# Optimization experiments

Measured on AMD Instinct MI355X. Metric: run time of the kernel, lower is better.

Reference implementation:

```python
import jax, jax.numpy as jnp
import numpy as np

HEAD_NUM = 16
SCALE = 1.0 / np.sqrt(HEAD_NUM)  # source divides by sqrt(head_num), not head_dim
MASK_VAL = -10000000.0


def setup_inputs() -> dict:
    key = jax.random.key(0)
    kq, kk, kv = jax.random.split(key, 3)
    shape = (2, 16, 2048, 64)  # [B, H, L, D]
    Q = jax.random.normal(kq, shape, dtype=jnp.float32)
    K = jax.random.normal(kk, shape, dtype=jnp.float32)
    V = jax.random.normal(kv, shape, dtype=jnp.float32)
    return {"Q": Q, "K": K, "V": V}


def reference(Q, K, V):
    L = Q.shape[-2]
    # [B, H, L, M] attention logits, scaled by 1/sqrt(head_num)
    logits = jnp.einsum('bhld,bhmd->bhlm', Q, K) * SCALE
    # causal mask: strictly-upper triangle gets -1e7 (additive, as in source)
    mask = jnp.triu(jnp.ones((L, L), dtype=logits.dtype), 1) * MASK_VAL
    logits = logits + mask[None, None, :, :]
    weights = jax.nn.softmax(logits, axis=-1)
    return jnp.einsum('bhlm,bhmd->bhld', weights, V)
```

## Files before the change

### kernel.cpp

```cpp
#include <hip/hip_runtime.h>
#include <hip/hip_bf16.h>

#define BM 128
#define BN 64
#define HD 64
#define LQ 2048
#define SD 72

typedef __attribute__((ext_vector_type(8))) short short8;
typedef __attribute__((ext_vector_type(4))) float f32x4;

#define QSCALE 0.360673760222241f

static __device__ __forceinline__ unsigned pk2(float a, float b) {
    union { __hip_bfloat162 h2; unsigned u; } c;
    c.h2 = __float22bfloat162_rn(make_float2(a, b));
    return c.u;
}

__global__ __launch_bounds__(512, 4)
void fa_fwd(const float* __restrict__ Qg,
            const float* __restrict__ Kg,
            const float* __restrict__ Vg,
            float* __restrict__ Og) {
    __shared__ unsigned short sQ[BM][SD];
    __shared__ unsigned short sK[2][BN][SD];
    __shared__ unsigned short sVt[2][HD][SD];
    __shared__ unsigned short sP[8][16][SD];

    const int t    = threadIdx.x;
    const int w    = t >> 6;
    const int lane = t & 63;
    const int qd   = lane >> 4;
    const int l    = lane & 15;

    const int bx  = blockIdx.x;
    const int idx = (bx >> 5) & 7;
    const int qt  = (bx & 256) ? idx : (15 - idx);
    const int bh  = bx & 31;
    const int q0  = qt * BM;

    const size_t base = (size_t)bh * (LQ * HD);
    const float* Qp = Qg + base + (size_t)q0 * HD;
    const float* Kp = Kg + base;
    const float* Vp = Vg + base;

    const int r0 = t >> 4;
    const int c4 = (t & 15) * 4;
    const int RA = w * 4;

#pragma unroll
    for (int p = 0; p < 4; ++p) {
        const int r = p * 32 + r0;
        const float4 v = *(const float4*)(Qp + (size_t)r * HD + c4);
        uint2 u;
        u.x = pk2(v.x * QSCALE, v.y * QSCALE);
        u.y = pk2(v.z * QSCALE, v.w * QSCALE);
        *(uint2*)&sQ[r][c4] = u;
    }

    float4 kA, kB, vA, vB;

    auto issue = [&](int kv0) {
        kA = *(const float4*)(Kp + (size_t)(kv0 + r0) * HD + c4);
        kB = *(const float4*)(Kp + (size_t)(kv0 + 32 + r0) * HD + c4);
        vA = *(const float4*)(Vp + (size_t)(kv0 + RA + qd) * HD + c4);
        vB = *(const float4*)(Vp + (size_t)(kv0 + 32 + RA + qd) * HD + c4);
    };

    auto vstore = [&](float4 vf, int R, int buf) {
        float e0 = vf.x, e1 = vf.y, e2 = vf.z, e3 = vf.w;
        float s0 = (qd & 2) ? e0 : e2;
        float s1 = (qd & 2) ? e1 : e3;
        s0 = __shfl_xor(s0, 32); s1 = __shfl_xor(s1, 32);
        if (qd & 2) { e0 = s0; e1 = s1; } else { e2 = s0; e3 = s1; }
        s0 = (qd & 1) ? e0 : e1;
        s1 = (qd & 1) ? e2 : e3;
        s0 = __shfl_xor(s0, 16); s1 = __shfl_xor(s1, 16);
        if (qd & 1) { e0 = s0; e2 = s1; } else { e1 = s0; e3 = s1; }
        const int d   = c4 + qd;
        const int col = ((((R >> 3) ^ (d >> 3)) & 7) << 3) | (R & 7);
        uint2 u; u.x = pk2(e0, e1); u.y = pk2(e2, e3);
        *(uint2*)&sVt[buf][d][col] = u;
    };

    auto commit = [&](int buf) {
        { uint2 u; u.x = pk2(kA.x, kA.y); u.y = pk2(kA.z, kA.w);
          *(uint2*)&sK[buf][r0][c4] = u; }
        { uint2 u; u.x = pk2(kB.x, kB.y); u.y = pk2(kB.z, kB.w);
          *(uint2*)&sK[buf][32 + r0][c4] = u; }
        vstore(vA, RA, buf);
        vstore(vB, 32 + RA, buf);
    };

    f32x4 accO[4];
#pragma unroll
    for (int mt = 0; mt < 4; ++mt) accO[mt] = (f32x4){0.f, 0.f, 0.f, 0.f};
    float lsum = 0.f;

    const int qrow  = q0 + w * 16 + l;
    const int qminw = q0 + w * 16;
    const int qmaxw = qminw + 15;
    const int n_it  = (q0 + BM) / BN;

    issue(0);
    commit(0);

    for (int it = 0; it < n_it; ++it) {
        const int kv0 = it * BN;
        const int buf = it & 1;
        __syncthreads();
        const bool more = (it + 1 < n_it);
        if (more) issue(kv0 + BN);

        if (kv0 <= qmaxw) {
            f32x4 accS[4];
#pragma unroll
            for (int mt = 0; mt < 4; ++mt) accS[mt] = (f32x4){0.f, 0.f, 0.f, 0.f};
#pragma unroll
            for (int ks = 0; ks < 2; ++ks) {
                const int ko = ks * 32 + qd * 8;
                const short8 bq = *(const short8*)&sQ[w * 16 + l][ko];
#pragma unroll
                for (int mt = 0; mt < 4; ++mt) {
                    const short8 ak = *(const short8*)&sK[buf][mt * 16 + l][ko];
                    accS[mt] = __builtin_amdgcn_mfma_f32_16x16x32_bf16(ak, bq, accS[mt], 0, 0, 0);
                }
            }

            if (kv0 + BN - 1 > qminw) {
#pragma unroll
                for (int mt = 0; mt < 4; ++mt) {
                    const int kvr = kv0 + mt * 16 + qd * 4;
#pragma unroll
                    for (int r = 0; r < 4; ++r)
                        if (kvr + r > qrow) accS[mt][r] = -1e30f;
                }
            }

#pragma unroll
            for (int mt = 0; mt < 4; ++mt) {
#pragma unroll
                for (int r = 0; r < 4; ++r) {
                    const float p = __builtin_amdgcn_exp2f(accS[mt][r]);
                    accS[mt][r] = p;
                    lsum += p;
                }
                uint2 u;
                u.x = pk2(accS[mt][0], accS[mt][1]);
                u.y = pk2(accS[mt][2], accS[mt][3]);
                *(uint2*)&sP[w][l][mt * 16 + qd * 4] = u;
            }
            asm volatile("s_waitcnt lgkmcnt(0)" ::: "memory");

            const int h = l >> 3;
#pragma unroll
            for (int ks = 0; ks < 2; ++ks) {
                const int ko = ks * 32 + qd * 8;
                const short8 bp = *(const short8*)&sP[w][l][ko];
#pragma unroll
                for (int mt = 0; mt < 4; ++mt) {
                    const int row = mt * 16 + l;
                    const int col = (((ks * 4 + qd) ^ (2 * mt + h)) & 7) << 3;
                    const short8 av = *(const short8*)&sVt[buf][row][col];
                    accO[mt] = __builtin_amdgcn_mfma_f32_16x16x32_bf16(av, bp, accO[mt], 0, 0, 0);
                }
            }
        }

        if (more) commit(buf ^ 1);
    }

    lsum += __shfl_xor(lsum, 16);
    lsum += __shfl_xor(lsum, 32);
    const float inv = 1.0f / lsum;
    float* Op = Og + base + (size_t)qrow * HD;
#pragma unroll
    for (int mt = 0; mt < 4; ++mt) {
        float4 o;
        o.x = accO[mt][0] * inv; o.y = accO[mt][1] * inv;
        o.z = accO[mt][2] * inv; o.w = accO[mt][3] * inv;
        *(float4*)(Op + mt * 16 + qd * 4) = o;
    }
}

extern "C" void kernel_launch(void* const* d_in, const int* in_sizes, int n_in,
                              void* d_out, int out_size, void* d_ws, size_t ws_size,
                              hipStream_t stream) {
    const float* Q = (const float*)d_in[0];
    const float* K = (const float*)d_in[1];
    const float* V = (const float*)d_in[2];
    float* O = (float*)d_out;
    fa_fwd<<<dim3(512), dim3(512), 0, stream>>>(Q, K, V, O);
}
```

Before: 124.2 us.

## Switch to 32x32x16 MFMA with 4 waves and Q in registers

```diff
diff --git a/kernel.cpp b/kernel.cpp
--- a/kernel.cpp
+++ b/kernel.cpp
@@ -5,12 +5,10 @@
 #define BN 64
 #define HD 64
 #define LQ 2048
-#define SD 72
+#define QSCALE 0.360673760222241f
 
 typedef __attribute__((ext_vector_type(8))) short short8;
-typedef __attribute__((ext_vector_type(4))) float f32x4;
-
-#define QSCALE 0.360673760222241f
+typedef __attribute__((ext_vector_type(16))) float f32x16;
 
 static __device__ __forceinline__ unsigned pk2(float a, float b) {
     union { __hip_bfloat162 h2; unsigned u; } c;
@@ -18,21 +16,24 @@
     return c.u;
 }
 
-__global__ __launch_bounds__(512, 4)
+static __device__ __forceinline__ int swz(int row, int oct) {
+    return (((row >> 3) ^ row) & 7) ^ oct;
+}
+
+__global__ __launch_bounds__(256, 3)
 void fa_fwd(const float* __restrict__ Qg,
             const float* __restrict__ Kg,
             const float* __restrict__ Vg,
             float* __restrict__ Og) {
-    __shared__ unsigned short sQ[BM][SD];
-    __shared__ unsigned short sK[2][BN][SD];
-    __shared__ unsigned short sVt[2][HD][SD];
-    __shared__ unsigned short sP[8][16][SD];
+    __shared__ unsigned short sK[2][BN][HD];
+    __shared__ unsigned short sVt[2][HD][BN];
+    __shared__ unsigned short sP[4][32][BN];
 
     const int t    = threadIdx.x;
     const int w    = t >> 6;
     const int lane = t & 63;
-    const int qd   = lane >> 4;
-    const int l    = lane & 15;
+    const int h    = lane >> 5;
+    const int l    = lane & 31;
 
     const int bx  = blockIdx.x;
     const int idx = (bx >> 5) & 7;
@@ -41,67 +42,80 @@
     const int q0  = qt * BM;
 
     const size_t base = (size_t)bh * (LQ * HD);
-    const float* Qp = Qg + base + (size_t)q0 * HD;
     const float* Kp = Kg + base;
     const float* Vp = Vg + base;
 
-    const int r0 = t >> 4;
-    const int c4 = (t & 15) * 4;
-    const int RA = w * 4;
-
-#pragma unroll
-    for (int p = 0; p < 4; ++p) {
-        const int r = p * 32 + r0;
-        const float4 v = *(const float4*)(Qp + (size_t)r * HD + c4);
-        uint2 u;
-        u.x = pk2(v.x * QSCALE, v.y * QSCALE);
-        u.y = pk2(v.z * QSCALE, v.w * QSCALE);
-        *(uint2*)&sQ[r][c4] = u;
+    const int qrow = q0 + w * 32 + l;
+
+    short8 bq[4];
+    {
+        const float* qp = Qg + base + (size_t)qrow * HD;
+#pragma unroll
+        for (int ks = 0; ks < 4; ++ks) {
+            const float4 a = *(const float4*)(qp + ks * 16 + h * 8);
+            const float4 b = *(const float4*)(qp + ks * 16 + h * 8 + 4);
+            union { short8 s; uint4 u; } cv;
+            cv.u.x = pk2(a.x * QSCALE, a.y * QSCALE);
+            cv.u.y = pk2(a.z * QSCALE, a.w * QSCALE);
+            cv.u.z = pk2(b.x * QSCALE, b.y * QSCALE);
+            cv.u.w = pk2(b.z * QSCALE, b.w * QSCALE);
+            bq[ks] = cv.s;
+        }
     }
 
-    float4 kA, kB, vA, vB;
-
+    const int kr   = t >> 4;
+    const int kc   = (t & 15) * 4;
+    const int ko   = (t & 15) >> 1;
+    const int koff = kc & 7;
+    const int vl   = lane & 15;
+    const int vqd  = lane >> 4;
+
+    float4 kf[4], vf[4];
     auto issue = [&](int kv0) {
-        kA = *(const float4*)(Kp + (size_t)(kv0 + r0) * HD + c4);
-        kB = *(const float4*)(Kp + (size_t)(kv0 + 32 + r0) * HD + c4);
-        vA = *(const float4*)(Vp + (size_t)(kv0 + RA + qd) * HD + c4);
-        vB = *(const float4*)(Vp + (size_t)(kv0 + 32 + RA + qd) * HD + c4);
+#pragma unroll
+        for (int p = 0; p < 4; ++p)
+            kf[p] = *(const float4*)(Kp + (size_t)(kv0 + p * 16 + kr) * HD + kc);
+#pragma unroll
+        for (int p = 0; p < 4; ++p)
+            vf[p] = *(const float4*)(Vp + (size_t)(kv0 + p * 16 + w * 4 + vqd) * HD + vl * 4);
     };
 
-    auto vstore = [&](float4 vf, int R, int buf) {
-        float e0 = vf.x, e1 = vf.y, e2 = vf.z, e3 = vf.w;
-        float s0 = (qd & 2) ? e0 : e2;
-        float s1 = (qd & 2) ? e1 : e3;
-        s0 = __shfl_xor(s0, 32); s1 = __shfl_xor(s1, 32);
-        if (qd & 2) { e0 = s0; e1 = s1; } else { e2 = s0; e3 = s1; }
-        s0 = (qd & 1) ? e0 : e1;
-        s1 = (qd & 1) ? e2 : e3;
-        s0 = __shfl_xor(s0, 16); s1 = __shfl_xor(s1, 16);
-        if (qd & 1) { e0 = s0; e2 = s1; } else { e1 = s0; e3 = s1; }
-        const int d   = c4 + qd;
-        const int col = ((((R >> 3) ^ (d >> 3)) & 7) << 3) | (R & 7);
-        uint2 u; u.x = pk2(e0, e1); u.y = pk2(e2, e3);
-        *(uint2*)&sVt[buf][d][col] = u;
+    auto commit = [&](int buf) {
+#pragma unroll
+        for (int p = 0; p < 4; ++p) {
+            const int r = p * 16 + kr;
+            uint2 u; u.x = pk2(kf[p].x, kf[p].y); u.y = pk2(kf[p].z, kf[p].w);
+            *(uint2*)&sK[buf][r][swz(r, ko) * 8 + koff] = u;
+        }
+#pragma unroll
+        for (int p = 0; p < 4; ++p) {
+            float e0 = vf[p].x, e1 = vf[p].y, e2 = vf[p].z, e3 = vf[p].w;
+            float s0 = (vqd & 2) ? e0 : e2;
+            float s1 = (vqd & 2) ? e1 : e3;
+            s0 = __shfl_xor(s0, 32); s1 = __shfl_xor(s1, 32);
+            if (vqd & 2) { e0 = s0; e1 = s1; } else { e2 = s0; e3 = s1; }
+            s0 = (vqd & 1) ? e0 : e1;
+            s1 = (vqd & 1) ? e2 : e3;
+            s0 = __shfl_xor(s0, 16); s1 = __shfl_xor(s1, 16);
+            if (vqd & 1) { e0 = s0; e2 = s1; } else { e1 = s0; e3 = s1; }
+            const int d = vl * 4 + vqd;
+            const int R = p * 16 + w * 4;
+            uint2 u; u.x = pk2(e0, e1); u.y = pk2(e2, e3);
+            *(uint2*)&sVt[buf][d][swz(d, R >> 3) * 8 + (R & 4)] = u;
+        }
     };
 
-    auto commit = [&](int buf) {
-        { uint2 u; u.x = pk2(kA.x, kA.y); u.y = pk2(kA.z, kA.w);
-          *(uint2*)&sK[buf][r0][c4] = u; }
-        { uint2 u; u.x = pk2(kB.x, kB.y); u.y = pk2(kB.z, kB.w);
-          *(uint2*)&sK[buf][32 + r0][c4] = u; }
-        vstore(vA, RA, buf);
-        vstore(vB, 32 + RA, buf);
-    };
-
-    f32x4 accO[4];
-#pragma unroll
-    for (int mt = 0; mt < 4; ++mt) accO[mt] = (f32x4){0.f, 0.f, 0.f, 0.f};
+    f32x16 accO[2];
+#pragma unroll
+    for (int mt = 0; mt < 2; ++mt)
+#pragma unroll
+        for (int i = 0; i < 16; ++i) accO[mt][i] = 0.f;
     float lsum = 0.f;
 
-    const int qrow  = q0 + w * 16 + l;
-    const int qminw = q0 + w * 16;
-    const int qmaxw = qminw + 15;
+    const int qminw = q0 + w * 32;
+    const int qmaxw = qminw + 31;
     const int n_it  = (q0 + BM) / BN;
+    const int swq   = ((l >> 3) ^ l) & 7;
 
     issue(0);
     commit(0);
@@ -114,74 +128,75 @@
         if (more) issue(kv0 + BN);
 
         if (kv0 <= qmaxw) {
-            f32x4 accS[4];
-#pragma unroll
-            for (int mt = 0; mt < 4; ++mt) accS[mt] = (f32x4){0.f, 0.f, 0.f, 0.f};
-#pragma unroll
-            for (int ks = 0; ks < 2; ++ks) {
-                const int ko = ks * 32 + qd * 8;
-                const short8 bq = *(const short8*)&sQ[w * 16 + l][ko];
-#pragma unroll
-                for (int mt = 0; mt < 4; ++mt) {
-                    const short8 ak = *(const short8*)&sK[buf][mt * 16 + l][ko];
-                    accS[mt] = __builtin_amdgcn_mfma_f32_16x16x32_bf16(ak, bq, accS[mt], 0, 0, 0);
+            f32x16 accS[2];
+#pragma unroll
+            for (int mt = 0; mt < 2; ++mt)
+#pragma unroll
+                for (int i = 0; i < 16; ++i) accS[mt][i] = 0.f;
+#pragma unroll
+            for (int ks = 0; ks < 4; ++ks) {
+#pragma unroll
+                for (int mt = 0; mt < 2; ++mt) {
+                    const int row = mt * 32 + l;
+                    const short8 ak = *(const short8*)&sK[buf][row][swz(row, 2 * ks + h) * 8];
+                    accS[mt] = __builtin_amdgcn_mfma_f32_32x32x16_bf16(ak, bq[ks], accS[mt], 0, 0, 0);
                 }
             }
 
             if (kv0 + BN - 1 > qminw) {
 #pragma unroll
-                for (int mt = 0; mt < 4; ++mt) {
-                    const int kvr = kv0 + mt * 16 + qd * 4;
-#pragma unroll
-                    for (int r = 0; r < 4; ++r)
-                        if (kvr + r > qrow) accS[mt][r] = -1e30f;
+                for (int mt = 0; mt < 2; ++mt)
+#pragma unroll
+                    for (int g = 0; g < 4; ++g)
+#pragma unroll
+                        for (int r = 0; r < 4; ++r)
+                            if (kv0 + mt * 32 + g * 8 + h * 4 + r > qrow)
+                                accS[mt][g * 4 + r] = -1e30f;
+            }
+
+#pragma unroll
+            for (int mt = 0; mt < 2; ++mt)
+#pragma unroll
+                for (int g = 0; g < 4; ++g) {
+                    const float p0 = __builtin_amdgcn_exp2f(accS[mt][g * 4 + 0]);
+                    const float p1 = __builtin_amdgcn_exp2f(accS[mt][g * 4 + 1]);
+                    const float p2 = __builtin_amdgcn_exp2f(accS[mt][g * 4 + 2]);
+                    const float p3 = __builtin_amdgcn_exp2f(accS[mt][g * 4 + 3]);
+                    lsum += (p0 + p1) + (p2 + p3);
+                    uint2 u; u.x = pk2(p0, p1); u.y = pk2(p2, p3);
+                    *(uint2*)&sP[w][l][(swq ^ (4 * mt + g)) * 8 + 4 * h] = u;
+                }
+            asm volatile("s_waitcnt lgkmcnt(0)" ::: "memory");
+
+#pragma unroll
+            for (int ks = 0; ks < 4; ++ks) {
+                const short8 bp = *(const short8*)&sP[w][l][(swq ^ (2 * ks + h)) * 8];
+#pragma unroll
+                for (int mt = 0; mt < 2; ++mt) {
+                    const int row = mt * 32 + l;
+                    const short8 av = *(const short8*)&sVt[buf][row][swz(row, 2 * ks + h) * 8];
+                    accO[mt] = __builtin_amdgcn_mfma_f32_32x32x16_bf16(av, bp, accO[mt], 0, 0, 0);
                 }
             }
-
-#pragma unroll
-            for (int mt = 0; mt < 4; ++mt) {
-#pragma unroll
-                for (int r = 0; r < 4; ++r) {
-                    const float p = __builtin_amdgcn_exp2f(accS[mt][r]);
-                    accS[mt][r] = p;
-                    lsum += p;
-                }
-                uint2 u;
-                u.x = pk2(accS[mt][0], accS[mt][1]);
-                u.y = pk2(accS[mt][2], accS[mt][3]);
-                *(uint2*)&sP[w][l][mt * 16 + qd * 4] = u;
-            }
-            asm volatile("s_waitcnt lgkmcnt(0)" ::: "memory");
-
-            const int h = l >> 3;
-#pragma unroll
-            for (int ks = 0; ks < 2; ++ks) {
-                const int ko = ks * 32 + qd * 8;
-                const short8 bp = *(const short8*)&sP[w][l][ko];
-#pragma unroll
-                for (int mt = 0; mt < 4; ++mt) {
-                    const int row = mt * 16 + l;
-                    const int col = (((ks * 4 + qd) ^ (2 * mt + h)) & 7) << 3;
-                    const short8 av = *(const short8*)&sVt[buf][row][col];
-                    accO[mt] = __builtin_amdgcn_mfma_f32_16x16x32_bf16(av, bp, accO[mt], 0, 0, 0);
-                }
-            }
         }
 
         if (more) commit(buf ^ 1);
     }
 
-    lsum += __shfl_xor(lsum, 16);
     lsum += __shfl_xor(lsum, 32);
     const float inv = 1.0f / lsum;
     float* Op = Og + base + (size_t)qrow * HD;
 #pragma unroll
-    for (int mt = 0; mt < 4; ++mt) {
-        float4 o;
-        o.x = accO[mt][0] * inv; o.y = accO[mt][1] * inv;
-        o.z = accO[mt][2] * inv; o.w = accO[mt][3] * inv;
-        *(float4*)(Op + mt * 16 + qd * 4) = o;
-    }
+    for (int mt = 0; mt < 2; ++mt)
+#pragma unroll
+        for (int g = 0; g < 4; ++g) {
+            float4 o;
+            o.x = accO[mt][g * 4 + 0] * inv;
+            o.y = accO[mt][g * 4 + 1] * inv;
+            o.z = accO[mt][g * 4 + 2] * inv;
+            o.w = accO[mt][g * 4 + 3] * inv;
+            *(float4*)(Op + mt * 32 + g * 8 + h * 4) = o;
+        }
 }
 
 extern "C" void kernel_launch(void* const* d_in, const int* in_sizes, int n_in,
@@ -191,5 +206,5 @@
     const float* K = (const float*)d_in[1];
     const float* V = (const float*)d_in[2];
     float* O = (float*)d_out;
-    fa_fwd<<<dim3(512), dim3(512), 0, stream>>>(Q, K, V, O);
-}
+    fa_fwd<<<dim3(512), dim3(256), 0, stream>>>(Q, K, V, O);
+}
```

Result: slower. 156.7 us (+26.2%).

## Keep Q in registers, XOR-swizzle unpadded LDS tiles, relax launch bounds

Applied to the files above, without the earlier changes.

```diff
diff --git a/kernel.cpp b/kernel.cpp
--- a/kernel.cpp
+++ b/kernel.cpp
@@ -5,12 +5,10 @@
 #define BN 64
 #define HD 64
 #define LQ 2048
-#define SD 72
+#define QSCALE 0.360673760222241f
 
 typedef __attribute__((ext_vector_type(8))) short short8;
 typedef __attribute__((ext_vector_type(4))) float f32x4;
-
-#define QSCALE 0.360673760222241f
 
 static __device__ __forceinline__ unsigned pk2(float a, float b) {
     union { __hip_bfloat162 h2; unsigned u; } c;
@@ -18,79 +16,86 @@
     return c.u;
 }
 
-__global__ __launch_bounds__(512, 4)
+__global__ __launch_bounds__(512, 2)
 void fa_fwd(const float* __restrict__ Qg,
             const float* __restrict__ Kg,
             const float* __restrict__ Vg,
             float* __restrict__ Og) {
-    __shared__ unsigned short sQ[BM][SD];
-    __shared__ unsigned short sK[2][BN][SD];
-    __shared__ unsigned short sVt[2][HD][SD];
-    __shared__ unsigned short sP[8][16][SD];
+    __shared__ unsigned short sK[2][BN][64];
+    __shared__ unsigned short sVt[2][HD][64];
+    __shared__ unsigned short sP[8][16][64];
 
     const int t    = threadIdx.x;
     const int w    = t >> 6;
     const int lane = t & 63;
     const int qd   = lane >> 4;
     const int l    = lane & 15;
+    const int l7   = l & 7;
 
     const int bx  = blockIdx.x;
-    const int idx = (bx >> 5) & 7;
-    const int qt  = (bx & 256) ? idx : (15 - idx);
+    const int qt  = 15 - (bx >> 5);
     const int bh  = bx & 31;
     const int q0  = qt * BM;
 
     const size_t base = (size_t)bh * (LQ * HD);
-    const float* Qp = Qg + base + (size_t)q0 * HD;
     const float* Kp = Kg + base;
     const float* Vp = Vg + base;
 
-    const int r0 = t >> 4;
-    const int c4 = (t & 15) * 4;
-    const int RA = w * 4;
+    const int qrow = q0 + w * 16 + l;
 
+    short8 bq[2];
+    {
+        const float* qp = Qg + base + (size_t)qrow * HD;
 #pragma unroll
-    for (int p = 0; p < 4; ++p) {
-        const int r = p * 32 + r0;
-        const float4 v = *(const float4*)(Qp + (size_t)r * HD + c4);
-        uint2 u;
-        u.x = pk2(v.x * QSCALE, v.y * QSCALE);
-        u.y = pk2(v.z * QSCALE, v.w * QSCALE);
-        *(uint2*)&sQ[r][c4] = u;
+        for (int ks = 0; ks < 2; ++ks) {
+            const float4 a = *(const float4*)(qp + ks * 32 + qd * 8);
+            const float4 b = *(const float4*)(qp + ks * 32 + qd * 8 + 4);
+            union { short8 s; uint4 u; } cv;
+            cv.u.x = pk2(a.x * QSCALE, a.y * QSCALE);
+            cv.u.y = pk2(a.z * QSCALE, a.w * QSCALE);
+            cv.u.z = pk2(b.x * QSCALE, b.y * QSCALE);
+            cv.u.w = pk2(b.z * QSCALE, b.w * QSCALE);
+            bq[ks] = cv.s;
+        }
     }
 
-    float4 kA, kB, vA, vB;
+    const int r0   = t >> 4;
+    const int c4   = (t & 15) * 4;
+    const int ko   = c4 >> 3;
+    const int koff = c4 & 7;
+    const int RA   = w * 4;
 
+    float4 kf[2], vf[2];
     auto issue = [&](int kv0) {
-        kA = *(const float4*)(Kp + (size_t)(kv0 + r0) * HD + c4);
-        kB = *(const float4*)(Kp + (size_t)(kv0 + 32 + r0) * HD + c4);
-        vA = *(const float4*)(Vp + (size_t)(kv0 + RA + qd) * HD + c4);
-        vB = *(const float4*)(Vp + (size_t)(kv0 + 32 + RA + qd) * HD + c4);
-    };
-
-    auto vstore = [&](float4 vf, int R, int buf) {
-        float e0 = vf.x, e1 = vf.y, e2 = vf.z, e3 = vf.w;
-        float s0 = (qd & 2) ? e0 : e2;
-        float s1 = (qd & 2) ? e1 : e3;
-        s0 = __shfl_xor(s0, 32); s1 = __shfl_xor(s1, 32);
-        if (qd & 2) { e0 = s0; e1 = s1; } else { e2 = s0; e3 = s1; }
-        s0 = (qd & 1) ? e0 : e1;
-        s1 = (qd & 1) ? e2 : e3;
-        s0 = __shfl_xor(s0, 16); s1 = __shfl_xor(s1, 16);
-        if (qd & 1) { e0 = s0; e2 = s1; } else { e1 = s0; e3 = s1; }
-        const int d   = c4 + qd;
-        const int col = ((((R >> 3) ^ (d >> 3)) & 7) << 3) | (R & 7);
-        uint2 u; u.x = pk2(e0, e1); u.y = pk2(e2, e3);
-        *(uint2*)&sVt[buf][d][col] = u;
+        kf[0] = *(const float4*)(Kp + (size_t)(kv0 + r0) * HD + c4);
+        kf[1] = *(const float4*)(Kp + (size_t)(kv0 + 32 + r0) * HD + c4);
+        vf[0] = *(const float4*)(Vp + (size_t)(kv0 + RA + qd) * HD + c4);
+        vf[1] = *(const float4*)(Vp + (size_t)(kv0 + 32 + RA + qd) * HD + c4);
     };
 
     auto commit = [&](int buf) {
-        { uint2 u; u.x = pk2(kA.x, kA.y); u.y = pk2(kA.z, kA.w);
-          *(uint2*)&sK[buf][r0][c4] = u; }
-        { uint2 u; u.x = pk2(kB.x, kB.y); u.y = pk2(kB.z, kB.w);
-          *(uint2*)&sK[buf][32 + r0][c4] = u; }
-        vstore(vA, RA, buf);
-        vstore(vB, 32 + RA, buf);
+#pragma unroll
+        for (int p = 0; p < 2; ++p) {
+            const int r = p * 32 + r0;
+            uint2 u; u.x = pk2(kf[p].x, kf[p].y); u.y = pk2(kf[p].z, kf[p].w);
+            *(uint2*)&sK[buf][r][((ko ^ (r & 7)) << 3) + koff] = u;
+        }
+#pragma unroll
+        for (int p = 0; p < 2; ++p) {
+            float e0 = vf[p].x, e1 = vf[p].y, e2 = vf[p].z, e3 = vf[p].w;
+            float s0 = (qd & 2) ? e0 : e2;
+            float s1 = (qd & 2) ? e1 : e3;
+            s0 = __shfl_xor(s0, 32); s1 = __shfl_xor(s1, 32);
+            if (qd & 2) { e0 = s0; e1 = s1; } else { e2 = s0; e3 = s1; }
+            s0 = (qd & 1) ? e0 : e1;
+            s1 = (qd & 1) ? e2 : e3;
+            s0 = __shfl_xor(s0, 16); s1 = __shfl_xor(s1, 16);
+            if (qd & 1) { e0 = s0; e2 = s1; } else { e1 = s0; e3 = s1; }
+            const int d = c4 + qd;
+            const int R = p * 32 + RA;
+            uint2 u; u.x = pk2(e0, e1); u.y = pk2(e2, e3);
+            *(uint2*)&sVt[buf][d][(((R >> 3) ^ (d & 7)) << 3) + (R & 4)] = u;
+        }
     };
 
     f32x4 accO[4];
@@ -98,7 +103,6 @@
     for (int mt = 0; mt < 4; ++mt) accO[mt] = (f32x4){0.f, 0.f, 0.f, 0.f};
     float lsum = 0.f;
 
-    const int qrow  = q0 + w * 16 + l;
     const int qminw = q0 + w * 16;
     const int qmaxw = qminw + 15;
     const int n_it  = (q0 + BM) / BN;
@@ -119,12 +123,12 @@
             for (int mt = 0; mt < 4; ++mt) accS[mt] = (f32x4){0.f, 0.f, 0.f, 0.f};
 #pragma unroll
             for (int ks = 0; ks < 2; ++ks) {
-                const int ko = ks * 32 + qd * 8;
-                const short8 bq = *(const short8*)&sQ[w * 16 + l][ko];
 #pragma unroll
                 for (int mt = 0; mt < 4; ++mt) {
-                    const short8 ak = *(const short8*)&sK[buf][mt * 16 + l][ko];
-                    accS[mt] = __builtin_amdgcn_mfma_f32_16x16x32_bf16(ak, bq, accS[mt], 0, 0, 0);
+                    const int row = mt * 16 + l;
+                    const short8 ak = *(const short8*)
+                        &sK[buf][row][(((ks * 4 + qd) ^ l7)) << 3];
+                    accS[mt] = __builtin_amdgcn_mfma_f32_16x16x32_bf16(ak, bq[ks], accS[mt], 0, 0, 0);
                 }
             }
 
@@ -140,29 +144,26 @@
 
 #pragma unroll
             for (int mt = 0; mt < 4; ++mt) {
-#pragma unroll
-                for (int r = 0; r < 4; ++r) {
-                    const float p = __builtin_amdgcn_exp2f(accS[mt][r]);
-                    accS[mt][r] = p;
-                    lsum += p;
-                }
-                uint2 u;
-                u.x = pk2(accS[mt][0], accS[mt][1]);
-                u.y = pk2(accS[mt][2], accS[mt][3]);
-                *(uint2*)&sP[w][l][mt * 16 + qd * 4] = u;
+                const float p0 = __builtin_amdgcn_exp2f(accS[mt][0]);
+                const float p1 = __builtin_amdgcn_exp2f(accS[mt][1]);
+                const float p2 = __builtin_amdgcn_exp2f(accS[mt][2]);
+                const float p3 = __builtin_amdgcn_exp2f(accS[mt][3]);
+                lsum += (p0 + p1) + (p2 + p3);
+                uint2 u; u.x = pk2(p0, p1); u.y = pk2(p2, p3);
+                const int oct = 2 * mt + (qd >> 1);
+                *(uint2*)&sP[w][l][((oct ^ l7) << 3) + ((qd & 1) << 2)] = u;
             }
             asm volatile("s_waitcnt lgkmcnt(0)" ::: "memory");
 
-            const int h = l >> 3;
 #pragma unroll
             for (int ks = 0; ks < 2; ++ks) {
-                const int ko = ks * 32 + qd * 8;
-                const short8 bp = *(const short8*)&sP[w][l][ko];
+                const short8 bp = *(const short8*)
+                    &sP[w][l][(((ks * 4 + qd) ^ l7)) << 3];
 #pragma unroll
                 for (int mt = 0; mt < 4; ++mt) {
                     const int row = mt * 16 + l;
-                    const int col = (((ks * 4 + qd) ^ (2 * mt + h)) & 7) << 3;
-                    const short8 av = *(const short8*)&sVt[buf][row][col];
+                    const short8 av = *(const short8*)
+                        &sVt[buf][row][(((ks * 4 + qd) ^ l7)) << 3];
                     accO[mt] = __builtin_amdgcn_mfma_f32_16x16x32_bf16(av, bp, accO[mt], 0, 0, 0);
                 }
             }
```

New measurement: 131.1 us. 5.6% more time.
